# Kernel optimization log

Hardware: AMD Instinct MI355X
Metric: run time of the kernel (lower is better)

## Reference

```python
import jax, jax.numpy as jnp
import numpy as np
import math

EMBED_DIM = 2048
NUM_Q_HEADS = 32
NUM_KV_HEADS = 8
HEAD_DIM = EMBED_DIM // NUM_Q_HEADS  # 64
GROUP = NUM_Q_HEADS // NUM_KV_HEADS  # 4
THETA = 10000.0


def _rope_tables(T, D):
    # matches torch.polar(ones, outer(pos, inv_freq)) -> cos/sin of shape (T, D//2)
    dim_half = D // 2
    inv_freq = 1.0 / (THETA ** (jnp.arange(dim_half, dtype=jnp.float32) / dim_half))
    freqs = jnp.arange(T, dtype=jnp.float32)[:, None] * inv_freq[None, :]  # (T, D//2)
    return jnp.cos(freqs), jnp.sin(freqs)


def _apply_rope(x, cos, sin):
    # x: (B, H, T, D); interleaved complex pairs along last dim, as in view_as_complex
    B, H, T, D = x.shape
    xp = x.reshape(B, H, T, D // 2, 2)
    xr, xi = xp[..., 0], xp[..., 1]
    c = cos[None, None, :, :]
    s = sin[None, None, :, :]
    or_ = xr * c - xi * s
    oi_ = xr * s + xi * c
    return jnp.stack([or_, oi_], axis=-1).reshape(B, H, T, D)


def setup_inputs() -> dict:
    key = jax.random.key(0)
    ks = jax.random.split(key, 5)
    B, T, C = 2, 2048, EMBED_DIM
    kvC = NUM_KV_HEADS * HEAD_DIM
    x = jax.random.normal(ks[0], (B, T, C), dtype=jnp.float32)
    Wq = jax.random.normal(ks[1], (C, C), dtype=jnp.float32) * 0.02
    Wk = jax.random.normal(ks[2], (kvC, C), dtype=jnp.float32) * 0.02
    Wv = jax.random.normal(ks[3], (kvC, C), dtype=jnp.float32) * 0.02
    Wo = jax.random.normal(ks[4], (C, C), dtype=jnp.float32) * 0.02
    return {"x": x, "Wq": Wq, "Wk": Wk, "Wv": Wv, "Wo": Wo}


def reference(x, Wq, Wk, Wv, Wo):
    B, T, C = x.shape
    Hq, Hkv, D, G = NUM_Q_HEADS, NUM_KV_HEADS, HEAD_DIM, GROUP
    scale = 1.0 / math.sqrt(D)

    q = (x @ Wq.T).reshape(B, T, Hq, D).transpose(0, 2, 1, 3)   # (B,Hq,T,D)
    k = (x @ Wk.T).reshape(B, T, Hkv, D).transpose(0, 2, 1, 3)  # (B,Hkv,T,D)
    v = (x @ Wv.T).reshape(B, T, Hkv, D).transpose(0, 2, 1, 3)

    cos, sin = _rope_tables(T, D)
    q = _apply_rope(q, cos, sin)
    k = _apply_rope(k, cos, sin)  # RoPE commutes with head repeat; same math

    # grouped attention: avoid materializing repeat_interleave of K/V
    qg = q.reshape(B, Hkv, G, T, D)
    att = jnp.einsum("bhgtd,bhsd->bhgts", qg, k) * scale  # (B,Hkv,G,T,T)

    causal = jnp.tril(jnp.ones((T, T), dtype=bool))
    att = jnp.where(causal[None, None, None, :, :], att, -jnp.inf)
    att = jax.nn.softmax(att, axis=-1)
    # dropout is identity in eval mode

    out = jnp.einsum("bhgts,bhsd->bhgtd", att, v)  # (B,Hkv,G,T,D)
    out = out.reshape(B, Hq, T, D).transpose(0, 2, 1, 3).reshape(B, T, C)
    return out @ Wo.T
```

## Files before the change

kernel.cpp:

```cpp
#include <hip/hip_runtime.h>
#include <hip/hip_bf16.h>
#include <math.h>

#define T_SEQ 2048
#define BATCH 2
#define CDIM  2048
#define HQ    32
#define HKV   8
#define HD    64
#define GRP   4
#define NQKV  3072

typedef __attribute__((ext_vector_type(8))) short  bf16x8;
typedef __attribute__((ext_vector_type(8))) ushort u16x8;
typedef __attribute__((ext_vector_type(4))) float  f32x4;

static __device__ __forceinline__ float bf2f(ushort u) {
    union { unsigned int ui; float f; } v; v.ui = ((unsigned int)u) << 16; return v.f;
}
static __device__ __forceinline__ ushort f2bf(float f) {
    union { float f; unsigned int ui; } v; v.f = f;
    unsigned int r = v.ui + 0x7FFFu + ((v.ui >> 16) & 1u);
    return (ushort)(r >> 16);
}
static __device__ __forceinline__ unsigned int pack2bf(float a, float b) {
    __hip_bfloat162 h = __float22bfloat162_rn(float2{a, b});
    union { __hip_bfloat162 h; unsigned int u; } v; v.h = h; return v.u;
}

__global__ void cvt_kernel(const float* __restrict__ in, ushort* __restrict__ out, long n) {
    long i = ((long)blockIdx.x * blockDim.x + threadIdx.x) * 8;
    if (i >= n) return;
    float4 a = *(const float4*)(in + i);
    float4 b = *(const float4*)(in + i + 4);
    u16x8 v;
    v[0] = f2bf(a.x); v[1] = f2bf(a.y); v[2] = f2bf(a.z); v[3] = f2bf(a.w);
    v[4] = f2bf(b.x); v[5] = f2bf(b.y); v[6] = f2bf(b.z); v[7] = f2bf(b.w);
    *(u16x8*)(out + i) = v;
}

template<bool F32OUT>
__global__ __launch_bounds__(256) void gemm_bt(const ushort* __restrict__ A,
                                               const ushort* __restrict__ B,
                                               void* __restrict__ C,
                                               int M, int N, int K) {
    __shared__ ushort As[128 * 64];
    __shared__ ushort Bs[128 * 64];
    const int tid  = threadIdx.x;
    const int wave = tid >> 6;
    const int lane = tid & 63;
    const int bm = blockIdx.x, bn = blockIdx.y;
    const int wm = wave >> 1, wn = wave & 1;

    f32x4 acc[4][4];
    #pragma unroll
    for (int i = 0; i < 4; ++i)
        #pragma unroll
        for (int j = 0; j < 4; ++j) { acc[i][j][0]=0.f; acc[i][j][1]=0.f; acc[i][j][2]=0.f; acc[i][j][3]=0.f; }

    const int r_sub  = tid >> 3;
    const int c_el   = (tid & 7) * 8;

    for (int k0 = 0; k0 < K; k0 += 64) {
        #pragma unroll
        for (int it = 0; it < 4; ++it) {
            int row = it * 32 + r_sub;
            const ushort* srcA = A + (size_t)(bm * 128 + row) * K + k0 + c_el;
            const ushort* srcB = B + (size_t)(bn * 128 + row) * K + k0 + c_el;
            __builtin_amdgcn_global_load_lds(
                (const __attribute__((address_space(1))) unsigned int*)srcA,
                (__attribute__((address_space(3))) unsigned int*)((char*)As + it * 4096 + wave * 1024),
                16, 0, 0);
            __builtin_amdgcn_global_load_lds(
                (const __attribute__((address_space(1))) unsigned int*)srcB,
                (__attribute__((address_space(3))) unsigned int*)((char*)Bs + it * 4096 + wave * 1024),
                16, 0, 0);
        }
        __syncthreads();

        const int lr = lane & 15;
        #pragma unroll
        for (int kk = 0; kk < 2; ++kk) {
            const int lk = kk * 32 + (lane >> 4) * 8;
            bf16x8 af[4], bfr[4];
            #pragma unroll
            for (int mi = 0; mi < 4; ++mi)
                af[mi] = *(const bf16x8*)&As[(wm * 64 + mi * 16 + lr) * 64 + lk];
            #pragma unroll
            for (int ni = 0; ni < 4; ++ni)
                bfr[ni] = *(const bf16x8*)&Bs[(wn * 64 + ni * 16 + lr) * 64 + lk];
            #pragma unroll
            for (int mi = 0; mi < 4; ++mi)
                #pragma unroll
                for (int ni = 0; ni < 4; ++ni)
                    acc[mi][ni] = __builtin_amdgcn_mfma_f32_16x16x32_bf16(af[mi], bfr[ni], acc[mi][ni], 0, 0, 0);
        }
        __syncthreads();
    }

    const int lr = lane & 15, lg = lane >> 4;
    #pragma unroll
    for (int mi = 0; mi < 4; ++mi)
        #pragma unroll
        for (int ni = 0; ni < 4; ++ni)
            #pragma unroll
            for (int r = 0; r < 4; ++r) {
                int row = bm * 128 + wm * 64 + mi * 16 + lg * 4 + r;
                int col = bn * 128 + wn * 64 + ni * 16 + lr;
                float v = acc[mi][ni][r];
                if (F32OUT) ((float*)C)[(size_t)row * N + col] = v;
                else        ((ushort*)C)[(size_t)row * N + col] = f2bf(v);
            }
}

__global__ void rope_qk(const ushort* __restrict__ qkv, ushort* __restrict__ Qh, ushort* __restrict__ Kh) {
    const int NQP = BATCH * T_SEQ * HQ * (HD / 2);
    int i = blockIdx.x * blockDim.x + threadIdx.x;
    if (i < NQP) {
        int row = i >> 10;
        int idx = i & 1023;
        int h = idx >> 5, j = idx & 31;
        int t = row & (T_SEQ - 1), b = row >> 11;
        const ushort* src = qkv + (size_t)row * NQKV + h * HD + 2 * j;
        unsigned int pin = *(const unsigned int*)src;
        float xr = bf2f((ushort)(pin & 0xFFFF));
        float xi = bf2f((ushort)(pin >> 16));
        float ang = (float)t * exp2f((float)j * -0.4152410118609203f);
        float c, s; sincosf(ang, &s, &c);
        float orr = xr * c - xi * s;
        float oi  = xr * s + xi * c;
        unsigned int pout = (unsigned int)f2bf(orr) | ((unsigned int)f2bf(oi) << 16);
        ushort* dst = Qh + ((size_t)((b * HQ + h) * T_SEQ + t)) * HD + 2 * j;
        *(unsigned int*)dst = pout;
    } else {
        int ii = i - NQP;
        int row = ii >> 8;
        int idx = ii & 255;
        int hk = idx >> 5, j = idx & 31;
        int t = row & (T_SEQ - 1), b = row >> 11;
        const ushort* src = qkv + (size_t)row * NQKV + CDIM + hk * HD + 2 * j;
        unsigned int pin = *(const unsigned int*)src;
        float xr = bf2f((ushort)(pin & 0xFFFF));
        float xi = bf2f((ushort)(pin >> 16));
        float ang = (float)t * exp2f((float)j * -0.4152410118609203f);
        float c, s; sincosf(ang, &s, &c);
        float orr = xr * c - xi * s;
        float oi  = xr * s + xi * c;
        unsigned int pout = (unsigned int)f2bf(orr) | ((unsigned int)f2bf(oi) << 16);
        ushort* dst = Kh + ((size_t)((b * HKV + hk) * T_SEQ + t)) * HD + 2 * j;
        *(unsigned int*)dst = pout;
    }
}

__global__ __launch_bounds__(256) void v_transpose(const ushort* __restrict__ qkv, ushort* __restrict__ Vt) {
    __shared__ ushort Vs[64][80];
    int bh = blockIdx.x;
    int tt = blockIdx.y;
    int b = bh >> 3, hk = bh & 7;
    int tid = threadIdx.x;
    #pragma unroll
    for (int c = 0; c < 2; ++c) {
        int rr = tid + c * 256;
        int tl = rr >> 3, d0 = (rr & 7) * 8;
        int row = b * T_SEQ + tt * 64 + tl;
        u16x8 v = *(const u16x8*)(qkv + (size_t)row * NQKV + CDIM + HKV * HD + hk * HD + d0);
        *(u16x8*)&Vs[tl][d0] = v;
    }
    __syncthreads();
    #pragma unroll
    for (int c = 0; c < 2; ++c) {
        int ch = tid + c * 256;
        int d = ch >> 3, t8 = (ch & 7) * 8;
        u16x8 o;
        #pragma unroll
        for (int j = 0; j < 8; ++j) o[j] = Vs[t8 + j][d];
        *(u16x8*)(Vt + ((size_t)(bh * HD + d)) * T_SEQ + tt * 64 + t8) = o;
    }
}

__global__ __launch_bounds__(256) void attn_kernel(const ushort* __restrict__ Qh,
                                                   const ushort* __restrict__ Kh,
                                                   const ushort* __restrict__ Vt,
                                                   ushort* __restrict__ O) {
    __shared__ ushort Ks[2][64 * 64];
    __shared__ ushort Vs[2][64 * 64];
    __shared__ ushort Ps[4][16 * 64];
    const int pairi = blockIdx.x, h = blockIdx.y, b = blockIdx.z;
    const int hk = h >> 2;
    const int tid = threadIdx.x, wave = tid >> 6, lane = tid & 63;
    const int lr = lane & 15, lg = lane >> 4;
    const float CEXP = 0.1803368801111204f;

    const ushort* Kbase = Kh + (size_t)(b * HKV + hk) * T_SEQ * HD;
    const ushort* Vbase = Vt + (size_t)(b * HKV + hk) * HD * T_SEQ;
    const int srow = tid >> 3, scol = (tid & 7) * 8;
    const int psw = (lr ^ (lr >> 3)) & 7;

    bf16x8 onesf;
    #pragma unroll
    for (int j = 0; j < 8; ++j) onesf[j] = (short)0x3F80;

    #pragma unroll
    for (int phalf = 0; phalf < 2; ++phalf) {
        const int qb = phalf ? (31 - pairi) : pairi;
        const ushort* Qbase = Qh + ((size_t)((b * HQ + h) * T_SEQ + qb * 64 + wave * 16 + lr)) * HD;
        bf16x8 qf[2];
        qf[0] = *(const bf16x8*)(Qbase + lg * 8);
        qf[1] = *(const bf16x8*)(Qbase + 32 + lg * 8);

        f32x4 oacc[4];
        #pragma unroll
        for (int dt = 0; dt < 4; ++dt) { oacc[dt][0]=0.f; oacc[dt][1]=0.f; oacc[dt][2]=0.f; oacc[dt][3]=0.f; }
        float l_r[4];
        #pragma unroll
        for (int r = 0; r < 4; ++r) l_r[r] = 0.f;
        float m_run = -INFINITY;

        const int q_glob = qb * 64 + wave * 16 + lr;
        const int nkt = qb + 1;

        u16x8 rK[2], rV[2];
        #pragma unroll
        for (int hh = 0; hh < 2; ++hh) {
            int r0 = srow + hh * 32;
            rK[hh] = *(const u16x8*)(Kbase + (size_t)r0 * HD + scol);
            rV[hh] = *(const u16x8*)(Vbase + (size_t)r0 * T_SEQ + scol);
        }
        __syncthreads();

        for (int kt = 0; kt < nkt; ++kt) {
            const int t0 = kt * 64;
            const int buf = kt & 1;
            #pragma unroll
            for (int hh = 0; hh < 2; ++hh) {
                int r0 = srow + hh * 32;
                int cb = (((tid & 7) ^ (r0 & 7))) * 8;
                *(u16x8*)&Ks[buf][r0 * 64 + cb] = rK[hh];
                *(u16x8*)&Vs[buf][r0 * 64 + cb] = rV[hh];
            }
            if (kt + 1 < nkt) {
                const int t1 = t0 + 64;
                #pragma unroll
                for (int hh = 0; hh < 2; ++hh) {
                    int r0 = srow + hh * 32;
                    rK[hh] = *(const u16x8*)(Kbase + (size_t)(t1 + r0) * HD + scol);
                    rV[hh] = *(const u16x8*)(Vbase + (size_t)r0 * T_SEQ + t1 + scol);
                }
            }
            __syncthreads();

            f32x4 sacc[4];
            #pragma unroll
            for (int ct = 0; ct < 4; ++ct) { sacc[ct][0]=0.f; sacc[ct][1]=0.f; sacc[ct][2]=0.f; sacc[ct][3]=0.f; }
            __builtin_amdgcn_s_setprio(1);
            #pragma unroll
            for (int kk = 0; kk < 2; ++kk) {
                #pragma unroll
                for (int ct = 0; ct < 4; ++ct) {
                    bf16x8 kf = *(const bf16x8*)&Ks[buf][(ct * 16 + lr) * 64 + (((kk * 4 + lg) ^ (lr & 7)) * 8)];
                    sacc[ct] = __builtin_amdgcn_mfma_f32_16x16x32_bf16(kf, qf[kk], sacc[ct], 0, 0, 0);
                }
            }
            __builtin_amdgcn_s_setprio(0);

            if (kt == qb) {
                #pragma unroll
                for (int ct = 0; ct < 4; ++ct) {
                    #pragma unroll
                    for (int r = 0; r < 4; ++r) {
                        int k_glob = t0 + ct * 16 + lg * 4 + r;
                        if (k_glob > q_glob) sacc[ct][r] = -INFINITY;
                    }
                }
            }

            float pm = sacc[0][0];
            #pragma unroll
            for (int ct = 0; ct < 4; ++ct)
                #pragma unroll
                for (int r = 0; r < 4; ++r) pm = fmaxf(pm, sacc[ct][r]);
            pm = fmaxf(pm, __shfl_xor(pm, 16));
            pm = fmaxf(pm, __shfl_xor(pm, 32));

            bool cskip = (pm <= m_run + 64.f);
            if (!__all(cskip)) {
                float mn = fmaxf(m_run, pm);
                float al = exp2f(CEXP * (m_run - mn));
                m_run = mn;
                #pragma unroll
                for (int r = 0; r < 4; ++r) {
                    float alq = __shfl(al, lg * 4 + r);
                    l_r[r] *= alq;
                    #pragma unroll
                    for (int dt = 0; dt < 4; ++dt) oacc[dt][r] *= alq;
                }
            }

            const float cm = CEXP * m_run;
            #pragma unroll
            for (int ct = 0; ct < 4; ++ct) {
                float p0 = exp2f(fmaf(CEXP, sacc[ct][0], -cm));
                float p1 = exp2f(fmaf(CEXP, sacc[ct][1], -cm));
                float p2 = exp2f(fmaf(CEXP, sacc[ct][2], -cm));
                float p3 = exp2f(fmaf(CEXP, sacc[ct][3], -cm));
                uint2 w; w.x = pack2bf(p0, p1); w.y = pack2bf(p2, p3);
                *(uint2*)&Ps[wave][lr * 64 + (((ct * 2 + (lg >> 1)) ^ psw) * 8) + (lg & 1) * 4] = w;
            }

            f32x4 lacc;
            lacc[0]=0.f; lacc[1]=0.f; lacc[2]=0.f; lacc[3]=0.f;
            __builtin_amdgcn_s_setprio(1);
            #pragma unroll
            for (int kk = 0; kk < 2; ++kk) {
                bf16x8 pf = *(const bf16x8*)&Ps[wave][lr * 64 + (((kk * 4 + lg) ^ psw) * 8)];
                lacc = __builtin_amdgcn_mfma_f32_16x16x32_bf16(pf, onesf, lacc, 0, 0, 0);
                #pragma unroll
                for (int dt = 0; dt < 4; ++dt) {
                    bf16x8 vf = *(const bf16x8*)&Vs[buf][(dt * 16 + lr) * 64 + (((kk * 4 + lg) ^ (lr & 7)) * 8)];
                    oacc[dt] = __builtin_amdgcn_mfma_f32_16x16x32_bf16(pf, vf, oacc[dt], 0, 0, 0);
                }
            }
            __builtin_amdgcn_s_setprio(0);
            #pragma unroll
            for (int r = 0; r < 4; ++r) l_r[r] += lacc[r];
        }

        #pragma unroll
        for (int dt = 0; dt < 4; ++dt)
            #pragma unroll
            for (int r = 0; r < 4; ++r) {
                int t = qb * 64 + wave * 16 + lg * 4 + r;
                int d = dt * 16 + lr;
                float v = oacc[dt][r] / l_r[r];
                O[((size_t)(b * T_SEQ + t)) * CDIM + h * HD + d] = f2bf(v);
            }
    }
}

extern "C" void kernel_launch(void* const* d_in, const int* in_sizes, int n_in,
                              void* d_out, int out_size, void* d_ws, size_t ws_size,
                              hipStream_t stream) {
    const float* x  = (const float*)d_in[0];
    const float* Wq = (const float*)d_in[1];
    const float* Wk = (const float*)d_in[2];
    const float* Wv = (const float*)d_in[3];
    const float* Wo = (const float*)d_in[4];
    float* out = (float*)d_out;

    ushort* xb    = (ushort*)d_ws;
    ushort* wqkvb = xb    + 8388608;
    ushort* wob   = wqkvb + 6291456;
    ushort* qkv   = wob   + 4194304;
    ushort* Qh    = qkv   + 12582912;
    ushort* Kh    = Qh    + 8388608;
    ushort* Vt    = Kh    + 2097152;
    ushort* attO  = xb;

    cvt_kernel<<<4096, 256, 0, stream>>>(x,  xb,    8388608);
    cvt_kernel<<<2048, 256, 0, stream>>>(Wq, wqkvb, 4194304);
    cvt_kernel<<< 512, 256, 0, stream>>>(Wk, wqkvb + 4194304, 1048576);
    cvt_kernel<<< 512, 256, 0, stream>>>(Wv, wqkvb + 5242880, 1048576);
    cvt_kernel<<<2048, 256, 0, stream>>>(Wo, wob,   4194304);

    gemm_bt<false><<<dim3(32, 24), 256, 0, stream>>>(xb, wqkvb, qkv, 4096, 3072, 2048);

    rope_qk<<<20480, 256, 0, stream>>>(qkv, Qh, Kh);
    v_transpose<<<dim3(16, 32), 256, 0, stream>>>(qkv, Vt);

    attn_kernel<<<dim3(16, 32, 2), 256, 0, stream>>>(Qh, Kh, Vt, attO);

    gemm_bt<true><<<dim3(32, 16), 256, 0, stream>>>(attO, wob, out, 4096, 2048, 2048);
}
```

Baseline: 364.8 us.

## Double-buffer GEMM LDS with XOR swizzle, XCD remap, and fused conversion launch

The GEMM now double-buffers its LDS tiles so the next K-tile's global-to-LDS load is issued while MFMAs run on the current tile. LDS columns are XOR-swizzled to cut bank conflicts, and workgroup IDs are remapped across the 8 XCDs for better L2 locality. s_setprio is raised around the MFMA block. The five fp32-to-bf16 conversion launches are merged into one kernel to save launch overhead. The trade-off is double the LDS per block (64KB), which can lower occupancy, and a single barrier per iteration, which makes the buffer reuse safety depend on ordering.

```diff
diff --git a/kernel.cpp b/kernel.cpp
--- a/kernel.cpp
+++ b/kernel.cpp
@@ -28,15 +28,25 @@
     union { __hip_bfloat162 h; unsigned int u; } v; v.h = h; return v.u;
 }
 
-__global__ void cvt_kernel(const float* __restrict__ in, ushort* __restrict__ out, long n) {
-    long i = ((long)blockIdx.x * blockDim.x + threadIdx.x) * 8;
-    if (i >= n) return;
-    float4 a = *(const float4*)(in + i);
-    float4 b = *(const float4*)(in + i + 4);
+__global__ void cvt5_kernel(const float* __restrict__ x,  const float* __restrict__ wq,
+                            const float* __restrict__ wk, const float* __restrict__ wv,
+                            const float* __restrict__ wo,
+                            ushort* __restrict__ xb, ushort* __restrict__ wqkvb,
+                            ushort* __restrict__ wob) {
+    long c = (long)blockIdx.x * blockDim.x + threadIdx.x;
+    const float* src; ushort* dst; long off;
+    if (c < 1048576L)      { src = x;  dst = xb;              off = c; }
+    else if (c < 1572864L) { src = wq; dst = wqkvb;           off = c - 1048576L; }
+    else if (c < 1703936L) { src = wk; dst = wqkvb + 4194304; off = c - 1572864L; }
+    else if (c < 1835008L) { src = wv; dst = wqkvb + 5242880; off = c - 1703936L; }
+    else                   { src = wo; dst = wob;             off = c - 1835008L; }
+    long i = off * 8;
+    float4 a = *(const float4*)(src + i);
+    float4 b = *(const float4*)(src + i + 4);
     u16x8 v;
     v[0] = f2bf(a.x); v[1] = f2bf(a.y); v[2] = f2bf(a.z); v[3] = f2bf(a.w);
     v[4] = f2bf(b.x); v[5] = f2bf(b.y); v[6] = f2bf(b.z); v[7] = f2bf(b.w);
-    *(u16x8*)(out + i) = v;
+    *(u16x8*)(dst + i) = v;
 }
 
 template<bool F32OUT>
@@ -44,12 +54,18 @@
                                                const ushort* __restrict__ B,
                                                void* __restrict__ C,
                                                int M, int N, int K) {
-    __shared__ ushort As[128 * 64];
-    __shared__ ushort Bs[128 * 64];
+    __shared__ ushort As[2][128 * 64];
+    __shared__ ushort Bs[2][128 * 64];
     const int tid  = threadIdx.x;
     const int wave = tid >> 6;
     const int lane = tid & 63;
-    const int bm = blockIdx.x, bn = blockIdx.y;
+
+    const int nbx = gridDim.x;
+    int wg = blockIdx.y * nbx + blockIdx.x;
+    const int nwg = nbx * gridDim.y;
+    const int cpx = nwg >> 3;
+    wg = (wg & 7) * cpx + (wg >> 3);
+    const int bm = wg % nbx, bn = wg / nbx;
     const int wm = wave >> 1, wn = wave & 1;
 
     f32x4 acc[4][4];
@@ -58,47 +74,56 @@
         #pragma unroll
         for (int j = 0; j < 4; ++j) { acc[i][j][0]=0.f; acc[i][j][1]=0.f; acc[i][j][2]=0.f; acc[i][j][3]=0.f; }
 
-    const int r_sub  = tid >> 3;
-    const int c_el   = (tid & 7) * 8;
-
-    for (int k0 = 0; k0 < K; k0 += 64) {
+    const int r_sub = tid >> 3;
+    const int c_src = (((tid & 7) ^ (r_sub & 7))) * 8;
+    const int lr = lane & 15, lg = lane >> 4;
+
+    const int nkt = K >> 6;
+
+    auto STAGE = [&](int k0, int db) {
         #pragma unroll
         for (int it = 0; it < 4; ++it) {
             int row = it * 32 + r_sub;
-            const ushort* srcA = A + (size_t)(bm * 128 + row) * K + k0 + c_el;
-            const ushort* srcB = B + (size_t)(bn * 128 + row) * K + k0 + c_el;
+            const ushort* srcA = A + (size_t)(bm * 128 + row) * K + k0 + c_src;
+            const ushort* srcB = B + (size_t)(bn * 128 + row) * K + k0 + c_src;
             __builtin_amdgcn_global_load_lds(
                 (const __attribute__((address_space(1))) unsigned int*)srcA,
-                (__attribute__((address_space(3))) unsigned int*)((char*)As + it * 4096 + wave * 1024),
+                (__attribute__((address_space(3))) unsigned int*)((char*)&As[db][0] + it * 4096 + wave * 1024),
                 16, 0, 0);
             __builtin_amdgcn_global_load_lds(
                 (const __attribute__((address_space(1))) unsigned int*)srcB,
-                (__attribute__((address_space(3))) unsigned int*)((char*)Bs + it * 4096 + wave * 1024),
+                (__attribute__((address_space(3))) unsigned int*)((char*)&Bs[db][0] + it * 4096 + wave * 1024),
                 16, 0, 0);
         }
-        __syncthreads();
-
-        const int lr = lane & 15;
+    };
+
+    STAGE(0, 0);
+    __syncthreads();
+
+    for (int t = 0; t < nkt; ++t) {
+        const int db = t & 1;
+        if (t + 1 < nkt) STAGE((t + 1) << 6, db ^ 1);
+
         #pragma unroll
         for (int kk = 0; kk < 2; ++kk) {
-            const int lk = kk * 32 + (lane >> 4) * 8;
             bf16x8 af[4], bfr[4];
             #pragma unroll
             for (int mi = 0; mi < 4; ++mi)
-                af[mi] = *(const bf16x8*)&As[(wm * 64 + mi * 16 + lr) * 64 + lk];
+                af[mi] = *(const bf16x8*)&As[db][(wm * 64 + mi * 16 + lr) * 64 + (((kk * 4 + lg) ^ (lr & 7)) * 8)];
             #pragma unroll
             for (int ni = 0; ni < 4; ++ni)
-                bfr[ni] = *(const bf16x8*)&Bs[(wn * 64 + ni * 16 + lr) * 64 + lk];
+                bfr[ni] = *(const bf16x8*)&Bs[db][(wn * 64 + ni * 16 + lr) * 64 + (((kk * 4 + lg) ^ (lr & 7)) * 8)];
+            __builtin_amdgcn_s_setprio(1);
             #pragma unroll
             for (int mi = 0; mi < 4; ++mi)
                 #pragma unroll
                 for (int ni = 0; ni < 4; ++ni)
                     acc[mi][ni] = __builtin_amdgcn_mfma_f32_16x16x32_bf16(af[mi], bfr[ni], acc[mi][ni], 0, 0, 0);
+            __builtin_amdgcn_s_setprio(0);
         }
         __syncthreads();
     }
 
-    const int lr = lane & 15, lg = lane >> 4;
     #pragma unroll
     for (int mi = 0; mi < 4; ++mi)
         #pragma unroll
@@ -356,11 +381,7 @@
     ushort* Vt    = Kh    + 2097152;
     ushort* attO  = xb;
 
-    cvt_kernel<<<4096, 256, 0, stream>>>(x,  xb,    8388608);
-    cvt_kernel<<<2048, 256, 0, stream>>>(Wq, wqkvb, 4194304);
-    cvt_kernel<<< 512, 256, 0, stream>>>(Wk, wqkvb + 4194304, 1048576);
-    cvt_kernel<<< 512, 256, 0, stream>>>(Wv, wqkvb + 5242880, 1048576);
-    cvt_kernel<<<2048, 256, 0, stream>>>(Wo, wob,   4194304);
+    cvt5_kernel<<<9216, 256, 0, stream>>>(x, Wq, Wk, Wv, Wo, xb, wqkvb, wob);
 
     gemm_bt<false><<<dim3(32, 24), 256, 0, stream>>>(xb, wqkvb, qkv, 4096, 3072, 2048);
 
```

After: 323.1 us. -11.4%, faster.
